# Optimization experiments

Hardware: AMD Instinct MI355X
Metric: run time of the kernel (lower is better)

Reference implementation:

```python
import jax, jax.numpy as jnp
import numpy as np

N = 100_000      # nodes
E = 1_600_000    # edges (avg degree 16)
IN, HID, OUT = 256, 256, 128  # in_dim, 2*out_dim, out_dim
BN_EPS = 1e-5


def setup_inputs() -> dict:
    key = jax.random.key(0)
    ks = jax.random.split(key, 8)
    x = jax.random.normal(ks[0], (N, IN), jnp.float32)
    edge_index = jax.random.randint(ks[1], (2, E), 0, N, dtype=jnp.int64)
    # GCNConv weights (glorot-ish scaling) + biases
    W1 = jax.random.normal(ks[2], (IN, HID), jnp.float32) * (1.0 / np.sqrt(IN))
    b1 = jnp.zeros((HID,), jnp.float32)
    W2 = jax.random.normal(ks[3], (HID, OUT), jnp.float32) * (1.0 / np.sqrt(HID))
    b2 = jnp.zeros((OUT,), jnp.float32)
    # BatchNorm1d affine params
    gamma = jnp.ones((HID,), jnp.float32)
    beta = jnp.zeros((HID,), jnp.float32)
    # PReLU single learnable slope (torch default 0.25)
    a = jnp.full((1,), 0.25, jnp.float32)
    return {"x": x, "edge_index": edge_index, "W1": W1, "b1": b1,
            "W2": W2, "b2": b2, "gamma": gamma, "beta": beta, "a": a}


def gcn_layer(x, W, b, src, dst):
    """GCNConv: h = D^-1/2 (A + I) D^-1/2 (x @ W) + b, self-loop weight 1."""
    h = x @ W                                           # [N, F]
    deg = jnp.zeros((N,), h.dtype).at[dst].add(1.0) + 1.0  # +1 self-loop
    dinv = jax.lax.rsqrt(deg)                           # [N]
    norm = dinv[src] * dinv[dst]                        # [E]
    agg = jnp.zeros_like(h).at[dst].add(h[src] * norm[:, None])
    agg = agg + h * (dinv * dinv)[:, None]              # self-loop term
    return agg + b


def reference(x, edge_index, W1, b1, W2, b2, gamma, beta, a):
    src, dst = edge_index[0], edge_index[1]
    h = gcn_layer(x, W1, b1, src, dst)                  # [N, HID]
    # BatchNorm1d (training mode: batch statistics, biased var)
    mean = jnp.mean(h, axis=0)
    var = jnp.var(h, axis=0)
    h = (h - mean) * jax.lax.rsqrt(var + BN_EPS) * gamma + beta
    # PReLU with single shared slope
    h = jnp.where(h > 0, h, a * h)
    return gcn_layer(h, W2, b2, src, dst)               # [N, OUT]
```

## Files before the change

kernel.cpp:

```cpp
#include <hip/hip_runtime.h>
#include <hip/hip_bf16.h>
#include <stdint.h>

#define IN_DIM 256

typedef __attribute__((ext_vector_type(8))) short short8;
typedef __attribute__((ext_vector_type(4))) float f32x4;

__device__ __forceinline__ float bf2f(unsigned short u){
  return __uint_as_float(((unsigned int)u) << 16);
}
__device__ __forceinline__ unsigned short f2bf(float f){
  unsigned int u = __float_as_uint(f);
  u = u + 0x7FFFu + ((u >> 16) & 1u);
  return (unsigned short)(u >> 16);
}
__device__ __forceinline__ int rfl(int v){ return __builtin_amdgcn_readfirstlane(v); }

#if __has_builtin(__builtin_amdgcn_cvt_f32_ubyte0)
__device__ __forceinline__ float ub0(uint v){ return __builtin_amdgcn_cvt_f32_ubyte0(v); }
__device__ __forceinline__ float ub1(uint v){ return __builtin_amdgcn_cvt_f32_ubyte1(v); }
__device__ __forceinline__ float ub2(uint v){ return __builtin_amdgcn_cvt_f32_ubyte2(v); }
__device__ __forceinline__ float ub3(uint v){ return __builtin_amdgcn_cvt_f32_ubyte3(v); }
#else
__device__ __forceinline__ float ub0(uint v){ return (float)(v & 0xFF); }
__device__ __forceinline__ float ub1(uint v){ return (float)((v >> 8) & 0xFF); }
__device__ __forceinline__ float ub2(uint v){ return (float)((v >> 16) & 0xFF); }
__device__ __forceinline__ float ub3(uint v){ return (float)(v >> 24); }
#endif

__global__ void k_detect(const void* ei, long long E, int N, int* flag){
  __shared__ int bad;
  if (threadIdx.x == 0) bad = 0;
  __syncthreads();
  const long long* p = (const long long*)ei;
  long long stride = E / 1024; if (stride < 1) stride = 1;
  for (int i = threadIdx.x; i < 1024; i += blockDim.x){
    long long idx = (long long)i * stride;
    if (idx >= E) break;
    long long v = p[idx];
    if (v < 0 || v >= (long long)N) atomicOr(&bad, 1);
  }
  __syncthreads();
  if (threadIdx.x == 0) flag[0] = bad ? 0 : 1;
}

__device__ __forceinline__ int edge_at(const void* ei, long long i, int f64){
  if (f64) return (int)((const long long*)ei)[i];
  return ((const int*)ei)[i];
}

__global__ void k_hist(const void* ei, long long E, const int* flag, int* cnt,
                       int* __restrict__ dst32, int* __restrict__ src32){
  long long e = (long long)blockIdx.x * blockDim.x + threadIdx.x;
  if (e < E){
    int f = flag[0];
    int s = edge_at(ei, e, f);
    int d = edge_at(ei, E + e, f);
    src32[e] = s;
    dst32[e] = d;
    atomicAdd(&cnt[d], 1);
  }
}

__global__ void k_scan1(const int* cnt, int* rs, int* bsum, float* dinv, int* fill, int N){
  __shared__ int sh[1024];
  int i = blockIdx.x * 1024 + threadIdx.x;
  int v = (i < N) ? cnt[i] : 0;
  sh[threadIdx.x] = v;
  __syncthreads();
  for (int o = 1; o < 1024; o <<= 1){
    int x = (threadIdx.x >= o) ? sh[threadIdx.x - o] : 0;
    __syncthreads();
    sh[threadIdx.x] += x;
    __syncthreads();
  }
  if (i < N){
    rs[i] = sh[threadIdx.x] - v;
    dinv[i] = rsqrtf((float)v + 1.0f);
    fill[i] = 0;
  }
  if (threadIdx.x == 1023) bsum[blockIdx.x] = sh[1023];
}

__global__ void k_scan2(const int* bsum, int* boff, int nb, int* rs, int N,
                        float* sums, float* sqs){
  __shared__ int sh[128];
  int t = threadIdx.x;
  int v = (t < nb) ? bsum[t] : 0;
  sh[t] = v;
  __syncthreads();
  for (int o = 1; o < 128; o <<= 1){
    int x = (t >= o) ? sh[t - o] : 0;
    __syncthreads();
    sh[t] += x;
    __syncthreads();
  }
  boff[t] = sh[t] - v;
  if (t == 127) rs[N] = sh[127];
  for (int j = t; j < 1024; j += 128){ sums[j] = 0.f; sqs[j] = 0.f; }
}

__global__ void k_scan3(int* rs, const int* boff, int N){
  int i = blockIdx.x * 1024 + threadIdx.x;
  if (i < N) rs[i] += boff[blockIdx.x];
}

__global__ __launch_bounds__(256) void k_scatter8(const int* __restrict__ dst32,
    const int* __restrict__ src32, long long E, const int* __restrict__ rs,
    int* __restrict__ fill, int* __restrict__ csrc, int N){
  const int g = blockIdx.x & 7;
  const int bg = blockIdx.x >> 3;
  const int Q = (N + 7) >> 3;
  const int lo = g * Q;
  const int hi = (lo + Q < N) ? lo + Q : N;
  const long long per = (E + 255) / 256;
  long long e0 = (long long)bg * per;
  long long e1 = e0 + per; if (e1 > E) e1 = E;
  for (long long e = e0 + threadIdx.x; e < e1; e += 256){
    int d = dst32[e];
    if (d >= lo && d < hi){
      int s = src32[e];
      int pos = atomicAdd(&fill[d], 1);
      csrc[rs[d] + pos] = s;
    }
  }
}

__global__ void k_prep(const float* __restrict__ x, ushort* __restrict__ xb,
                       const float* __restrict__ W1, ushort* __restrict__ W1t,
                       const float* __restrict__ W2, ushort* __restrict__ W2t,
                       int N, int NP){
  int idx = blockIdx.x * 256 + threadIdx.x;
  int nxq = NP * 64;
  if (idx < nxq){
    int row = idx >> 6, q = idx & 63;
    ushort4 o = {0, 0, 0, 0};
    if (row < N){
      float4 v = ((const float4*)x)[(size_t)row * 64 + q];
      o.x = f2bf(v.x); o.y = f2bf(v.y); o.z = f2bf(v.z); o.w = f2bf(v.w);
    }
    ((ushort4*)xb)[idx] = o;
  } else {
    int j = idx - nxq;
    if (j < 256 * 256){
      int n = j >> 8, k = j & 255;
      W1t[j] = f2bf(W1[(size_t)k * 256 + n]);
    } else {
      j -= 65536;
      if (j < 128 * 256){
        int n = j >> 8, k = j & 255;
        W2t[j] = f2bf(W2[(size_t)k * 128 + n]);
      }
    }
  }
}

__global__ __launch_bounds__(256, 2) void k_gemm1q(const ushort* __restrict__ A,
    const ushort* __restrict__ Bt, unsigned char* __restrict__ q8,
    float* __restrict__ sc1, const float* __restrict__ dinv, int N){
  __shared__ ushort As[128 * 64];
  __shared__ ushort Bs[256 * 64];
  __shared__ float smax[4][64];
  const int tid = threadIdx.x;
  const int wave = tid >> 6, lane = tid & 63;
  const long long row0 = (long long)blockIdx.x * 128;
  const int lr = lane >> 3, lc = lane & 7;
  const int mrow = ((wave & 1) << 6) + (lane & 15);
  const int ncb = ((wave >> 1) << 7) + (lane & 15);

  f32x4 acc[4][8];
  #pragma unroll
  for (int i = 0; i < 4; ++i)
    #pragma unroll
    for (int j = 0; j < 8; ++j)
      acc[i][j] = (f32x4){0.f, 0.f, 0.f, 0.f};

  const ushort* gA = A + (row0 + wave * 32 + lr) * 256 + lc * 8;
  const ushort* gB = Bt + (wave * 64 + lr) * 256 + lc * 8;
  ushort* lA = As + wave * 2048;
  ushort* lB = Bs + wave * 4096;

  #pragma unroll
  for (int kt = 0; kt < 4; ++kt){
    #pragma unroll
    for (int i = 0; i < 4; ++i)
      __builtin_amdgcn_global_load_lds(
          (const __attribute__((address_space(1))) void*)(gA + kt * 64 + i * 8 * 256),
          (__attribute__((address_space(3))) void*)(lA + i * 512), 16, 0, 0);
    #pragma unroll
    for (int i = 0; i < 8; ++i)
      __builtin_amdgcn_global_load_lds(
          (const __attribute__((address_space(1))) void*)(gB + kt * 64 + i * 8 * 256),
          (__attribute__((address_space(3))) void*)(lB + i * 512), 16, 0, 0);
    __syncthreads();
    #pragma unroll
    for (int ks = 0; ks < 2; ++ks){
      const int kb = ks * 32 + ((lane >> 4) << 3);
      short8 af[4], bfv[8];
      #pragma unroll
      for (int i = 0; i < 4; ++i) af[i] = *(const short8*)(As + (mrow + i * 16) * 64 + kb);
      #pragma unroll
      for (int j = 0; j < 8; ++j) bfv[j] = *(const short8*)(Bs + (ncb + j * 16) * 64 + kb);
      #pragma unroll
      for (int i = 0; i < 4; ++i)
        #pragma unroll
        for (int j = 0; j < 8; ++j)
          acc[i][j] = __builtin_amdgcn_mfma_f32_16x16x32_bf16(af[i], bfv[j], acc[i][j], 0, 0, 0);
    }
    __syncthreads();
  }

  const int rbase = ((wave & 1) << 6) + ((lane >> 4) << 2);
  float m[4][4];
  #pragma unroll
  for (int i = 0; i < 4; ++i)
    #pragma unroll
    for (int r = 0; r < 4; ++r){
      long long row = row0 + rbase + i * 16 + r;
      float dv = (row < N) ? dinv[row] : 0.f;
      float mm = 0.f;
      #pragma unroll
      for (int j = 0; j < 8; ++j){
        float v = dv * acc[i][j][r];
        acc[i][j][r] = v;
        mm = fmaxf(mm, fabsf(v));
      }
      #pragma unroll
      for (int o = 8; o >= 1; o >>= 1) mm = fmaxf(mm, __shfl_xor(mm, o, 16));
      m[i][r] = mm;
    }
  if ((lane & 15) == 0){
    #pragma unroll
    for (int i = 0; i < 4; ++i)
      #pragma unroll
      for (int r = 0; r < 4; ++r)
        smax[wave][((lane >> 4) << 2) + i * 16 + r] = m[i][r];
  }
  __syncthreads();
  #pragma unroll
  for (int i = 0; i < 4; ++i)
    #pragma unroll
    for (int r = 0; r < 4; ++r){
      int rh = ((lane >> 4) << 2) + i * 16 + r;
      long long row = row0 + ((wave & 1) << 6) + rh;
      float mm = fmaxf(m[i][r], smax[wave ^ 2][rh]);
      float inv = (mm > 0.f) ? 127.0f / mm : 0.f;
      if (wave < 2 && (lane & 15) == 0 && row < N) sc1[row] = mm * (1.0f / 127.0f);
      #pragma unroll
      for (int j = 0; j < 8; ++j){
        unsigned char b = (unsigned char)(int)(rintf(acc[i][j][r] * inv) + 128.0f);
        q8[(size_t)row * 256 + ncb + j * 16] = b;
      }
    }
}

__global__ __launch_bounds__(256) void k_gemm2q(const ushort* __restrict__ A,
    const ushort* __restrict__ Bt, unsigned char* __restrict__ q8,
    float* __restrict__ sc2, const float* __restrict__ dinv, int N){
  __shared__ ushort As[128 * 64];
  __shared__ ushort Bs[128 * 64];
  __shared__ float smax[4][64];
  const int tid = threadIdx.x;
  const int wave = tid >> 6, lane = tid & 63;
  const long long row0 = (long long)blockIdx.x * 128;
  const int lr = lane >> 3, lc = lane & 7;
  const int mrow = ((wave & 1) << 6) + (lane & 15);
  const int ncol = ((wave >> 1) << 6) + (lane & 15);

  f32x4 acc[4][4];
  #pragma unroll
  for (int i = 0; i < 4; ++i)
    #pragma unroll
    for (int j = 0; j < 4; ++j)
      acc[i][j] = (f32x4){0.f, 0.f, 0.f, 0.f};

  const ushort* gA = A + (row0 + wave * 32 + lr) * 256 + lc * 8;
  const ushort* gB = Bt + ((long long)(wave * 32 + lr)) * 256 + lc * 8;
  ushort* lA = As + wave * 2048;
  ushort* lB = Bs + wave * 2048;

  #pragma unroll
  for (int kt = 0; kt < 4; ++kt){
    #pragma unroll
    for (int i = 0; i < 4; ++i){
      __builtin_amdgcn_global_load_lds(
          (const __attribute__((address_space(1))) void*)(gA + kt * 64 + i * 8 * 256),
          (__attribute__((address_space(3))) void*)(lA + i * 512), 16, 0, 0);
      __builtin_amdgcn_global_load_lds(
          (const __attribute__((address_space(1))) void*)(gB + kt * 64 + i * 8 * 256),
          (__attribute__((address_space(3))) void*)(lB + i * 512), 16, 0, 0);
    }
    __syncthreads();
    #pragma unroll
    for (int ks = 0; ks < 2; ++ks){
      const int kb = ks * 32 + ((lane >> 4) << 3);
      short8 af[4], bfv[4];
      #pragma unroll
      for (int i = 0; i < 4; ++i) af[i] = *(const short8*)(As + (mrow + i * 16) * 64 + kb);
      #pragma unroll
      for (int j = 0; j < 4; ++j) bfv[j] = *(const short8*)(Bs + (ncol + j * 16) * 64 + kb);
      #pragma unroll
      for (int i = 0; i < 4; ++i)
        #pragma unroll
        for (int j = 0; j < 4; ++j)
          acc[i][j] = __builtin_amdgcn_mfma_f32_16x16x32_bf16(af[i], bfv[j], acc[i][j], 0, 0, 0);
    }
    __syncthreads();
  }

  const int rbase = ((wave & 1) << 6) + ((lane >> 4) << 2);
  const int cb = ((wave >> 1) << 6) + (lane & 15);
  float m[4][4];
  #pragma unroll
  for (int i = 0; i < 4; ++i)
    #pragma unroll
    for (int r = 0; r < 4; ++r){
      long long row = row0 + rbase + i * 16 + r;
      float dv = (row < N) ? dinv[row] : 0.f;
      float mm = 0.f;
      #pragma unroll
      for (int j = 0; j < 4; ++j){
        float v = dv * acc[i][j][r];
        acc[i][j][r] = v;
        mm = fmaxf(mm, fabsf(v));
      }
      #pragma unroll
      for (int o = 8; o >= 1; o >>= 1) mm = fmaxf(mm, __shfl_xor(mm, o, 16));
      m[i][r] = mm;
    }
  if ((lane & 15) == 0){
    #pragma unroll
    for (int i = 0; i < 4; ++i)
      #pragma unroll
      for (int r = 0; r < 4; ++r)
        smax[wave][((lane >> 4) << 2) + i * 16 + r] = m[i][r];
  }
  __syncthreads();
  #pragma unroll
  for (int i = 0; i < 4; ++i)
    #pragma unroll
    for (int r = 0; r < 4; ++r){
      int rh = ((lane >> 4) << 2) + i * 16 + r;
      long long row = row0 + ((wave & 1) << 6) + rh;
      float mm = fmaxf(m[i][r], smax[wave ^ 2][rh]);
      float inv = (mm > 0.f) ? 127.0f / mm : 0.f;
      if (wave < 2 && (lane & 15) == 0 && row < N) sc2[row] = mm * (1.0f / 127.0f);
      #pragma unroll
      for (int j = 0; j < 4; ++j){
        unsigned char b = (unsigned char)(int)(rintf(acc[i][j][r] * inv) + 128.0f);
        q8[(size_t)row * 128 + cb + j * 16] = b;
      }
    }
}

__global__ __launch_bounds__(256) void k_agg1(const uint* __restrict__ q, const float* __restrict__ sc,
    const int* __restrict__ rs, const int* __restrict__ csrc, const float* __restrict__ b1,
    ushort* __restrict__ h1, float* __restrict__ sums, float* __restrict__ sqs,
    int N, int nblocks){
  __shared__ float red[4 * 512];
  const int lane = threadIdx.x & 63;
  const int wid = rfl((blockIdx.x * 256 + threadIdx.x) >> 6);
  const int nw = (nblocks * 256) >> 6;
  const float4 bb = ((const float4*)b1)[lane];
  const uint* ql = q + lane;
  float st0 = 0.f, st1 = 0.f, st2 = 0.f, st3 = 0.f;
  float sq0 = 0.f, sq1 = 0.f, sq2 = 0.f, sq3 = 0.f;

  for (int n = wid; n < N; n += nw){
    int e = rfl(rs[n]), end = rfl(rs[n + 1]);
    float dn = rsqrtf((float)(end - e) + 1.0f);
    float scn = sc[n];
    uint v = ql[(uint)n << 6];
    float ssum = scn;
    float a0 = scn * ub0(v), a1 = scn * ub1(v), a2 = scn * ub2(v), a3 = scn * ub3(v);
    for (; e + 8 <= end; e += 8){
      int s0 = rfl(csrc[e]),     s1 = rfl(csrc[e + 1]), s2 = rfl(csrc[e + 2]), s3 = rfl(csrc[e + 3]);
      int s4 = rfl(csrc[e + 4]), s5 = rfl(csrc[e + 5]), s6 = rfl(csrc[e + 6]), s7 = rfl(csrc[e + 7]);
      float c0 = sc[s0], c1 = sc[s1], c2 = sc[s2], c3 = sc[s3];
      float c4 = sc[s4], c5 = sc[s5], c6 = sc[s6], c7 = sc[s7];
      uint v0 = ql[(uint)s0 << 6];
      uint v1 = ql[(uint)s1 << 6];
      uint v2 = ql[(uint)s2 << 6];
      uint v3 = ql[(uint)s3 << 6];
      uint v4 = ql[(uint)s4 << 6];
      uint v5 = ql[(uint)s5 << 6];
      uint v6 = ql[(uint)s6 << 6];
      uint v7 = ql[(uint)s7 << 6];
      ssum += ((c0 + c1) + (c2 + c3)) + ((c4 + c5) + (c6 + c7));
      a0 += ((c0 * ub0(v0) + c1 * ub0(v1)) + (c2 * ub0(v2) + c3 * ub0(v3)))
          + ((c4 * ub0(v4) + c5 * ub0(v5)) + (c6 * ub0(v6) + c7 * ub0(v7)));
      a1 += ((c0 * ub1(v0) + c1 * ub1(v1)) + (c2 * ub1(v2) + c3 * ub1(v3)))
          + ((c4 * ub1(v4) + c5 * ub1(v5)) + (c6 * ub1(v6) + c7 * ub1(v7)));
      a2 += ((c0 * ub2(v0) + c1 * ub2(v1)) + (c2 * ub2(v2) + c3 * ub2(v3)))
          + ((c4 * ub2(v4) + c5 * ub2(v5)) + (c6 * ub2(v6) + c7 * ub2(v7)));
      a3 += ((c0 * ub3(v0) + c1 * ub3(v1)) + (c2 * ub3(v2) + c3 * ub3(v3)))
          + ((c4 * ub3(v4) + c5 * ub3(v5)) + (c6 * ub3(v6) + c7 * ub3(v7)));
    }
    for (; e + 4 <= end; e += 4){
      int s0 = rfl(csrc[e]), s1 = rfl(csrc[e + 1]), s2 = rfl(csrc[e + 2]), s3 = rfl(csrc[e + 3]);
      float c0 = sc[s0], c1 = sc[s1], c2 = sc[s2], c3 = sc[s3];
      uint v0 = ql[(uint)s0 << 6];
      uint v1 = ql[(uint)s1 << 6];
      uint v2 = ql[(uint)s2 << 6];
      uint v3 = ql[(uint)s3 << 6];
      ssum += (c0 + c1) + (c2 + c3);
      a0 += (c0 * ub0(v0) + c1 * ub0(v1)) + (c2 * ub0(v2) + c3 * ub0(v3));
      a1 += (c0 * ub1(v0) + c1 * ub1(v1)) + (c2 * ub1(v2) + c3 * ub1(v3));
      a2 += (c0 * ub2(v0) + c1 * ub2(v1)) + (c2 * ub2(v2) + c3 * ub2(v3));
      a3 += (c0 * ub3(v0) + c1 * ub3(v1)) + (c2 * ub3(v2) + c3 * ub3(v3));
    }
    for (; e < end; ++e){
      int s = rfl(csrc[e]);
      float c = sc[s];
      uint vv = ql[(uint)s << 6];
      ssum += c;
      a0 += c * ub0(vv); a1 += c * ub1(vv); a2 += c * ub2(vv); a3 += c * ub3(vv);
    }
    float corr = -128.0f * ssum;
    float h0 = dn * (a0 + corr) + bb.x;
    float h1v = dn * (a1 + corr) + bb.y;
    float h2 = dn * (a2 + corr) + bb.z;
    float h3 = dn * (a3 + corr) + bb.w;
    st0 += h0; st1 += h1v; st2 += h2; st3 += h3;
    sq0 += h0 * h0; sq1 += h1v * h1v; sq2 += h2 * h2; sq3 += h3 * h3;
    ushort4 o;
    o.x = f2bf(h0); o.y = f2bf(h1v); o.z = f2bf(h2); o.w = f2bf(h3);
    ((ushort4*)h1)[(size_t)n * 64 + lane] = o;
  }

  int wv = threadIdx.x >> 6;
  int f = lane * 4;
  red[wv * 512 + f]     = st0; red[wv * 512 + f + 1] = st1;
  red[wv * 512 + f + 2] = st2; red[wv * 512 + f + 3] = st3;
  __syncthreads();
  float v0s = red[threadIdx.x] + red[512 + threadIdx.x] + red[1024 + threadIdx.x] + red[1536 + threadIdx.x];
  __syncthreads();
  red[wv * 512 + f]     = sq0; red[wv * 512 + f + 1] = sq1;
  red[wv * 512 + f + 2] = sq2; red[wv * 512 + f + 3] = sq3;
  __syncthreads();
  float v0q = red[threadIdx.x] + red[512 + threadIdx.x] + red[1024 + threadIdx.x] + red[1536 + threadIdx.x];
  if (threadIdx.x < 256){
    int rep = ((blockIdx.x & 3) << 8) + threadIdx.x;
    atomicAdd(&sums[rep], v0s);
    atomicAdd(&sqs[rep], v0q);
  }
}

__global__ __launch_bounds__(256) void k_agg2(const ushort* __restrict__ q, const float* __restrict__ sc,
    const int* __restrict__ rs, const int* __restrict__ csrc, const float* __restrict__ b2,
    float* __restrict__ out, int N, int nblocks){
  const int lane = threadIdx.x & 63;
  const int wid = rfl((blockIdx.x * 256 + threadIdx.x) >> 6);
  const int nw = (nblocks * 256) >> 6;
  const float2 bb = ((const float2*)b2)[lane];
  const ushort* ql = q + lane;

  for (int n = wid; n < N; n += nw){
    int e = rfl(rs[n]), end = rfl(rs[n + 1]);
    float dn = rsqrtf((float)(end - e) + 1.0f);
    float scn = sc[n];
    uint v = (uint)ql[(uint)n << 6];
    float ssum = scn;
    float a0 = scn * ub0(v), a1 = scn * ub1(v);
    for (; e + 8 <= end; e += 8){
      int s0 = rfl(csrc[e]),     s1 = rfl(csrc[e + 1]), s2 = rfl(csrc[e + 2]), s3 = rfl(csrc[e + 3]);
      int s4 = rfl(csrc[e + 4]), s5 = rfl(csrc[e + 5]), s6 = rfl(csrc[e + 6]), s7 = rfl(csrc[e + 7]);
      float c0 = sc[s0], c1 = sc[s1], c2 = sc[s2], c3 = sc[s3];
      float c4 = sc[s4], c5 = sc[s5], c6 = sc[s6], c7 = sc[s7];
      uint v0 = (uint)ql[(uint)s0 << 6];
      uint v1 = (uint)ql[(uint)s1 << 6];
      uint v2 = (uint)ql[(uint)s2 << 6];
      uint v3 = (uint)ql[(uint)s3 << 6];
      uint v4 = (uint)ql[(uint)s4 << 6];
      uint v5 = (uint)ql[(uint)s5 << 6];
      uint v6 = (uint)ql[(uint)s6 << 6];
      uint v7 = (uint)ql[(uint)s7 << 6];
      ssum += ((c0 + c1) + (c2 + c3)) + ((c4 + c5) + (c6 + c7));
      a0 += ((c0 * ub0(v0) + c1 * ub0(v1)) + (c2 * ub0(v2) + c3 * ub0(v3)))
          + ((c4 * ub0(v4) + c5 * ub0(v5)) + (c6 * ub0(v6) + c7 * ub0(v7)));
      a1 += ((c0 * ub1(v0) + c1 * ub1(v1)) + (c2 * ub1(v2) + c3 * ub1(v3)))
          + ((c4 * ub1(v4) + c5 * ub1(v5)) + (c6 * ub1(v6) + c7 * ub1(v7)));
    }
    for (; e + 4 <= end; e += 4){
      int s0 = rfl(csrc[e]), s1 = rfl(csrc[e + 1]), s2 = rfl(csrc[e + 2]), s3 = rfl(csrc[e + 3]);
      float c0 = sc[s0], c1 = sc[s1], c2 = sc[s2], c3 = sc[s3];
      uint v0 = (uint)ql[(uint)s0 << 6];
      uint v1 = (uint)ql[(uint)s1 << 6];
      uint v2 = (uint)ql[(uint)s2 << 6];
      uint v3 = (uint)ql[(uint)s3 << 6];
      ssum += (c0 + c1) + (c2 + c3);
      a0 += (c0 * ub0(v0) + c1 * ub0(v1)) + (c2 * ub0(v2) + c3 * ub0(v3));
      a1 += (c0 * ub1(v0) + c1 * ub1(v1)) + (c2 * ub1(v2) + c3 * ub1(v3));
    }
    for (; e < end; ++e){
      int s = rfl(csrc[e]);
      float c = sc[s];
      uint vv = (uint)ql[(uint)s << 6];
      ssum += c;
      a0 += c * ub0(vv); a1 += c * ub1(vv);
    }
    float corr = -128.0f * ssum;
    float2 r;
    r.x = dn * (a0 + corr) + bb.x;
    r.y = dn * (a1 + corr) + bb.y;
    ((float2*)out)[(size_t)n * 64 + lane] = r;
  }
}

__global__ void k_prelu(const ushort* __restrict__ h1, const float* __restrict__ sums,
                        const float* __restrict__ sqs, const float* __restrict__ gamma,
                        const float* __restrict__ beta, const float* __restrict__ aP,
                        ushort* __restrict__ P, int N, int NP){
  int idx = blockIdx.x * 256 + threadIdx.x;
  int row = idx >> 7, cp = idx & 127;
  if (row >= NP) return;
  uint o = 0;
  if (row < N){
    int c0 = 2 * cp;
    float inv = 1.0f / (float)N;
    float s0 = sums[c0]     + sums[256 + c0]     + sums[512 + c0]     + sums[768 + c0];
    float s1 = sums[c0 + 1] + sums[256 + c0 + 1] + sums[512 + c0 + 1] + sums[768 + c0 + 1];
    float q0 = sqs[c0]      + sqs[256 + c0]      + sqs[512 + c0]      + sqs[768 + c0];
    float q1 = sqs[c0 + 1]  + sqs[256 + c0 + 1]  + sqs[512 + c0 + 1]  + sqs[768 + c0 + 1];
    float m0 = s0 * inv,     m1 = s1 * inv;
    float v0 = q0 * inv - m0 * m0, v1 = q1 * inv - m1 * m1;
    float sc0 = gamma[c0] * rsqrtf(v0 + 1e-5f);
    float sc1 = gamma[c0 + 1] * rsqrtf(v1 + 1e-5f);
    float sh0 = beta[c0] - m0 * sc0;
    float sh1 = beta[c0 + 1] - m1 * sc1;
    uint v = ((const uint*)h1)[(size_t)row * 128 + cp];
    float aa = aP[0];
    float x0 = bf2f((unsigned short)(v & 0xFFFF)) * sc0 + sh0;
    float x1 = bf2f((unsigned short)(v >> 16)) * sc1 + sh1;
    x0 = x0 > 0.f ? x0 : aa * x0;
    x1 = x1 > 0.f ? x1 : aa * x1;
    o = (uint)f2bf(x0) | ((uint)f2bf(x1) << 16);
  }
  ((uint*)P)[idx] = o;
}

extern "C" void kernel_launch(void* const* d_in, const int* in_sizes, int n_in,
                              void* d_out, int out_size, void* d_ws, size_t ws_size,
                              hipStream_t stream){
  const float* x  = (const float*)d_in[0];
  const void*  ei = d_in[1];
  const float* W1 = (const float*)d_in[2];
  const float* b1 = (const float*)d_in[3];
  const float* W2 = (const float*)d_in[4];
  const float* b2 = (const float*)d_in[5];
  const float* gm = (const float*)d_in[6];
  const float* bt = (const float*)d_in[7];
  const float* aP = (const float*)d_in[8];
  float* out = (float*)d_out;

  const int N = in_sizes[0] / IN_DIM;
  const long long E = in_sizes[1] / 2;
  const int NP = ((N + 127) / 128) * 128;

  char* w = (char*)d_ws;
  size_t off = 0;
  auto carve = [&](size_t bytes) -> char* {
    char* p = w + off;
    off += (bytes + 255) & ~(size_t)255;
    return p;
  };
  ushort* xb  = (ushort*)carve((size_t)NP * 256 * 2);
  ushort* hb  = (ushort*)carve((size_t)NP * 256 * 2);
  ushort* h1b = (ushort*)carve((size_t)NP * 256 * 2);
  ushort* W1t = (ushort*)carve(256 * 256 * 2);
  ushort* W2t = (ushort*)carve(128 * 256 * 2);
  int*   cnt  = (int*)  carve((size_t)N * 4);
  int*   rs   = (int*)  carve((size_t)(N + 1) * 4);
  int*   fill = (int*)  carve((size_t)N * 4);
  int*   csrc = (int*)  carve((size_t)E * 4);
  float* dinv = (float*)carve((size_t)N * 4);
  float* sc1  = (float*)carve((size_t)N * 4);
  float* sc2  = (float*)carve((size_t)N * 4);
  int*   bsum = (int*)  carve(512);
  int*   boff = (int*)  carve(512);
  float* sums = (float*)carve(4096);
  float* sqs  = (float*)carve(4096);
  int*   flag = (int*)  carve(256);
  int*   dst32 = (int*)hb;
  int*   src32 = ((int*)hb) + E;
  uint*   q8a = (uint*)hb;
  ushort* q8b = (ushort*)h1b;

  const int NB1 = (N + 1023) / 1024;
  const int egrid = (int)((E + 255) / 256);
  const int prep_grid = (NP * 64 + 256 * 256 + 128 * 256 + 255) / 256;
  const int AGG1_BLOCKS = 2048, AGG2_BLOCKS = 2048;

  k_detect<<<1, 256, 0, stream>>>(ei, E, N, flag);
  hipMemsetAsync(cnt, 0, (size_t)N * 4, stream);
  k_prep<<<prep_grid, 256, 0, stream>>>(x, xb, W1, W1t, W2, W2t, N, NP);
  k_hist<<<egrid, 256, 0, stream>>>(ei, E, flag, cnt, dst32, src32);
  k_scan1<<<NB1, 1024, 0, stream>>>(cnt, rs, bsum, dinv, fill, N);
  k_scan2<<<1, 128, 0, stream>>>(bsum, boff, NB1, rs, N, sums, sqs);
  k_scan3<<<NB1, 1024, 0, stream>>>(rs, boff, N);
  k_scatter8<<<2048, 256, 0, stream>>>(dst32, src32, E, rs, fill, csrc, N);

  k_gemm1q<<<NP / 128, 256, 0, stream>>>(xb, W1t, (unsigned char*)q8a, sc1, dinv, N);
  k_agg1<<<AGG1_BLOCKS, 256, 0, stream>>>(q8a, sc1, rs, csrc, b1, h1b, sums, sqs, N, AGG1_BLOCKS);
  k_prelu<<<(NP * 128 + 255) / 256, 256, 0, stream>>>(h1b, sums, sqs, gm, bt, aP, xb, N, NP);
  k_gemm2q<<<NP / 128, 256, 0, stream>>>(xb, W2t, (unsigned char*)q8b, sc2, dinv, N);
  k_agg2<<<AGG2_BLOCKS, 256, 0, stream>>>(q8b, sc2, rs, csrc, b2, out, N, AGG2_BLOCKS);
}
```

Baseline: 580.9 us.

## Fuse fp32-to-bf16 conversion of x into GEMM1 and use FMA chains in aggregation

```diff
diff --git a/kernel.cpp b/kernel.cpp
--- a/kernel.cpp
+++ b/kernel.cpp
@@ -127,36 +127,22 @@
   }
 }
 
-__global__ void k_prep(const float* __restrict__ x, ushort* __restrict__ xb,
-                       const float* __restrict__ W1, ushort* __restrict__ W1t,
-                       const float* __restrict__ W2, ushort* __restrict__ W2t,
-                       int N, int NP){
-  int idx = blockIdx.x * 256 + threadIdx.x;
-  int nxq = NP * 64;
-  if (idx < nxq){
-    int row = idx >> 6, q = idx & 63;
-    ushort4 o = {0, 0, 0, 0};
-    if (row < N){
-      float4 v = ((const float4*)x)[(size_t)row * 64 + q];
-      o.x = f2bf(v.x); o.y = f2bf(v.y); o.z = f2bf(v.z); o.w = f2bf(v.w);
-    }
-    ((ushort4*)xb)[idx] = o;
+__global__ void k_prepw(const float* __restrict__ W1, ushort* __restrict__ W1t,
+                        const float* __restrict__ W2, ushort* __restrict__ W2t){
+  int j = blockIdx.x * 256 + threadIdx.x;
+  if (j < 256 * 256){
+    int n = j >> 8, k = j & 255;
+    W1t[j] = f2bf(W1[(size_t)k * 256 + n]);
   } else {
-    int j = idx - nxq;
-    if (j < 256 * 256){
-      int n = j >> 8, k = j & 255;
-      W1t[j] = f2bf(W1[(size_t)k * 256 + n]);
-    } else {
-      j -= 65536;
-      if (j < 128 * 256){
-        int n = j >> 8, k = j & 255;
-        W2t[j] = f2bf(W2[(size_t)k * 128 + n]);
-      }
-    }
-  }
-}
-
-__global__ __launch_bounds__(256, 2) void k_gemm1q(const ushort* __restrict__ A,
+    int j2 = j - 65536;
+    if (j2 < 128 * 256){
+      int n = j2 >> 8, k = j2 & 255;
+      W2t[j2] = f2bf(W2[(size_t)k * 128 + n]);
+    }
+  }
+}
+
+__global__ __launch_bounds__(256, 2) void k_gemm1q(const float* __restrict__ X,
     const ushort* __restrict__ Bt, unsigned char* __restrict__ q8,
     float* __restrict__ sc1, const float* __restrict__ dinv, int N){
   __shared__ ushort As[128 * 64];
@@ -166,6 +152,7 @@
   const int wave = tid >> 6, lane = tid & 63;
   const long long row0 = (long long)blockIdx.x * 128;
   const int lr = lane >> 3, lc = lane & 7;
+  const int sr = lane >> 4, scq = lane & 15;
   const int mrow = ((wave & 1) << 6) + (lane & 15);
   const int ncb = ((wave >> 1) << 7) + (lane & 15);
 
@@ -176,23 +163,27 @@
     for (int j = 0; j < 8; ++j)
       acc[i][j] = (f32x4){0.f, 0.f, 0.f, 0.f};
 
-  const ushort* gA = A + (row0 + wave * 32 + lr) * 256 + lc * 8;
   const ushort* gB = Bt + (wave * 64 + lr) * 256 + lc * 8;
-  ushort* lA = As + wave * 2048;
   ushort* lB = Bs + wave * 4096;
 
   #pragma unroll
   for (int kt = 0; kt < 4; ++kt){
-    #pragma unroll
-    for (int i = 0; i < 4; ++i)
-      __builtin_amdgcn_global_load_lds(
-          (const __attribute__((address_space(1))) void*)(gA + kt * 64 + i * 8 * 256),
-          (__attribute__((address_space(3))) void*)(lA + i * 512), 16, 0, 0);
     #pragma unroll
     for (int i = 0; i < 8; ++i)
       __builtin_amdgcn_global_load_lds(
           (const __attribute__((address_space(1))) void*)(gB + kt * 64 + i * 8 * 256),
           (__attribute__((address_space(3))) void*)(lB + i * 512), 16, 0, 0);
+    #pragma unroll
+    for (int p = 0; p < 8; ++p){
+      int rl = wave * 32 + p * 4 + sr;
+      long long grow = row0 + rl;
+      float4 xv = {0.f, 0.f, 0.f, 0.f};
+      if (grow < N) xv = *(const float4*)(X + grow * 256 + kt * 64 + scq * 4);
+      uint2 wv;
+      wv.x = (uint)f2bf(xv.x) | ((uint)f2bf(xv.y) << 16);
+      wv.y = (uint)f2bf(xv.z) | ((uint)f2bf(xv.w) << 16);
+      *(uint2*)(As + rl * 64 + scq * 4) = wv;
+    }
     __syncthreads();
     #pragma unroll
     for (int ks = 0; ks < 2; ++ks){
@@ -388,14 +379,22 @@
       uint v6 = ql[(uint)s6 << 6];
       uint v7 = ql[(uint)s7 << 6];
       ssum += ((c0 + c1) + (c2 + c3)) + ((c4 + c5) + (c6 + c7));
-      a0 += ((c0 * ub0(v0) + c1 * ub0(v1)) + (c2 * ub0(v2) + c3 * ub0(v3)))
-          + ((c4 * ub0(v4) + c5 * ub0(v5)) + (c6 * ub0(v6) + c7 * ub0(v7)));
-      a1 += ((c0 * ub1(v0) + c1 * ub1(v1)) + (c2 * ub1(v2) + c3 * ub1(v3)))
-          + ((c4 * ub1(v4) + c5 * ub1(v5)) + (c6 * ub1(v6) + c7 * ub1(v7)));
-      a2 += ((c0 * ub2(v0) + c1 * ub2(v1)) + (c2 * ub2(v2) + c3 * ub2(v3)))
-          + ((c4 * ub2(v4) + c5 * ub2(v5)) + (c6 * ub2(v6) + c7 * ub2(v7)));
-      a3 += ((c0 * ub3(v0) + c1 * ub3(v1)) + (c2 * ub3(v2) + c3 * ub3(v3)))
-          + ((c4 * ub3(v4) + c5 * ub3(v5)) + (c6 * ub3(v6) + c7 * ub3(v7)));
+      a0 = fmaf(c0, ub0(v0), a0); a0 = fmaf(c1, ub0(v1), a0);
+      a0 = fmaf(c2, ub0(v2), a0); a0 = fmaf(c3, ub0(v3), a0);
+      a0 = fmaf(c4, ub0(v4), a0); a0 = fmaf(c5, ub0(v5), a0);
+      a0 = fmaf(c6, ub0(v6), a0); a0 = fmaf(c7, ub0(v7), a0);
+      a1 = fmaf(c0, ub1(v0), a1); a1 = fmaf(c1, ub1(v1), a1);
+      a1 = fmaf(c2, ub1(v2), a1); a1 = fmaf(c3, ub1(v3), a1);
+      a1 = fmaf(c4, ub1(v4), a1); a1 = fmaf(c5, ub1(v5), a1);
+      a1 = fmaf(c6, ub1(v6), a1); a1 = fmaf(c7, ub1(v7), a1);
+      a2 = fmaf(c0, ub2(v0), a2); a2 = fmaf(c1, ub2(v1), a2);
+      a2 = fmaf(c2, ub2(v2), a2); a2 = fmaf(c3, ub2(v3), a2);
+      a2 = fmaf(c4, ub2(v4), a2); a2 = fmaf(c5, ub2(v5), a2);
+      a2 = fmaf(c6, ub2(v6), a2); a2 = fmaf(c7, ub2(v7), a2);
+      a3 = fmaf(c0, ub3(v0), a3); a3 = fmaf(c1, ub3(v1), a3);
+      a3 = fmaf(c2, ub3(v2), a3); a3 = fmaf(c3, ub3(v3), a3);
+      a3 = fmaf(c4, ub3(v4), a3); a3 = fmaf(c5, ub3(v5), a3);
+      a3 = fmaf(c6, ub3(v6), a3); a3 = fmaf(c7, ub3(v7), a3);
     }
     for (; e + 4 <= end; e += 4){
       int s0 = rfl(csrc[e]), s1 = rfl(csrc[e + 1]), s2 = rfl(csrc[e + 2]), s3 = rfl(csrc[e + 3]);
@@ -405,17 +404,22 @@
       uint v2 = ql[(uint)s2 << 6];
       uint v3 = ql[(uint)s3 << 6];
       ssum += (c0 + c1) + (c2 + c3);
-      a0 += (c0 * ub0(v0) + c1 * ub0(v1)) + (c2 * ub0(v2) + c3 * ub0(v3));
-      a1 += (c0 * ub1(v0) + c1 * ub1(v1)) + (c2 * ub1(v2) + c3 * ub1(v3));
-      a2 += (c0 * ub2(v0) + c1 * ub2(v1)) + (c2 * ub2(v2) + c3 * ub2(v3));
-      a3 += (c0 * ub3(v0) + c1 * ub3(v1)) + (c2 * ub3(v2) + c3 * ub3(v3));
+      a0 = fmaf(c0, ub0(v0), a0); a0 = fmaf(c1, ub0(v1), a0);
+      a0 = fmaf(c2, ub0(v2), a0); a0 = fmaf(c3, ub0(v3), a0);
+      a1 = fmaf(c0, ub1(v0), a1); a1 = fmaf(c1, ub1(v1), a1);
+      a1 = fmaf(c2, ub1(v2), a1); a1 = fmaf(c3, ub1(v3), a1);
+      a2 = fmaf(c0, ub2(v0), a2); a2 = fmaf(c1, ub2(v1), a2);
+      a2 = fmaf(c2, ub2(v2), a2); a2 = fmaf(c3, ub2(v3), a2);
+      a3 = fmaf(c0, ub3(v0), a3); a3 = fmaf(c1, ub3(v1), a3);
+      a3 = fmaf(c2, ub3(v2), a3); a3 = fmaf(c3, ub3(v3), a3);
     }
     for (; e < end; ++e){
       int s = rfl(csrc[e]);
       float c = sc[s];
       uint vv = ql[(uint)s << 6];
       ssum += c;
-      a0 += c * ub0(vv); a1 += c * ub1(vv); a2 += c * ub2(vv); a3 += c * ub3(vv);
+      a0 = fmaf(c, ub0(vv), a0); a1 = fmaf(c, ub1(vv), a1);
+      a2 = fmaf(c, ub2(vv), a2); a3 = fmaf(c, ub3(vv), a3);
     }
     float corr = -128.0f * ssum;
     float h0 = dn * (a0 + corr) + bb.x;
@@ -477,10 +481,14 @@
       uint v6 = (uint)ql[(uint)s6 << 6];
       uint v7 = (uint)ql[(uint)s7 << 6];
       ssum += ((c0 + c1) + (c2 + c3)) + ((c4 + c5) + (c6 + c7));
-      a0 += ((c0 * ub0(v0) + c1 * ub0(v1)) + (c2 * ub0(v2) + c3 * ub0(v3)))
-          + ((c4 * ub0(v4) + c5 * ub0(v5)) + (c6 * ub0(v6) + c7 * ub0(v7)));
-      a1 += ((c0 * ub1(v0) + c1 * ub1(v1)) + (c2 * ub1(v2) + c3 * ub1(v3)))
-          + ((c4 * ub1(v4) + c5 * ub1(v5)) + (c6 * ub1(v6) + c7 * ub1(v7)));
+      a0 = fmaf(c0, ub0(v0), a0); a0 = fmaf(c1, ub0(v1), a0);
+      a0 = fmaf(c2, ub0(v2), a0); a0 = fmaf(c3, ub0(v3), a0);
+      a0 = fmaf(c4, ub0(v4), a0); a0 = fmaf(c5, ub0(v5), a0);
+      a0 = fmaf(c6, ub0(v6), a0); a0 = fmaf(c7, ub0(v7), a0);
+      a1 = fmaf(c0, ub1(v0), a1); a1 = fmaf(c1, ub1(v1), a1);
+      a1 = fmaf(c2, ub1(v2), a1); a1 = fmaf(c3, ub1(v3), a1);
+      a1 = fmaf(c4, ub1(v4), a1); a1 = fmaf(c5, ub1(v5), a1);
+      a1 = fmaf(c6, ub1(v6), a1); a1 = fmaf(c7, ub1(v7), a1);
     }
     for (; e + 4 <= end; e += 4){
       int s0 = rfl(csrc[e]), s1 = rfl(csrc[e + 1]), s2 = rfl(csrc[e + 2]), s3 = rfl(csrc[e + 3]);
@@ -490,15 +498,17 @@
       uint v2 = (uint)ql[(uint)s2 << 6];
       uint v3 = (uint)ql[(uint)s3 << 6];
       ssum += (c0 + c1) + (c2 + c3);
-      a0 += (c0 * ub0(v0) + c1 * ub0(v1)) + (c2 * ub0(v2) + c3 * ub0(v3));
-      a1 += (c0 * ub1(v0) + c1 * ub1(v1)) + (c2 * ub1(v2) + c3 * ub1(v3));
+      a0 = fmaf(c0, ub0(v0), a0); a0 = fmaf(c1, ub0(v1), a0);
+      a0 = fmaf(c2, ub0(v2), a0); a0 = fmaf(c3, ub0(v3), a0);
+      a1 = fmaf(c0, ub1(v0), a1); a1 = fmaf(c1, ub1(v1), a1);
+      a1 = fmaf(c2, ub1(v2), a1); a1 = fmaf(c3, ub1(v3), a1);
     }
     for (; e < end; ++e){
       int s = rfl(csrc[e]);
       float c = sc[s];
       uint vv = (uint)ql[(uint)s << 6];
       ssum += c;
-      a0 += c * ub0(vv); a1 += c * ub1(vv);
+      a0 = fmaf(c, ub0(vv), a0); a1 = fmaf(c, ub1(vv), a1);
     }
     float corr = -128.0f * ssum;
     float2 r;
@@ -589,19 +599,18 @@
 
   const int NB1 = (N + 1023) / 1024;
   const int egrid = (int)((E + 255) / 256);
-  const int prep_grid = (NP * 64 + 256 * 256 + 128 * 256 + 255) / 256;
   const int AGG1_BLOCKS = 2048, AGG2_BLOCKS = 2048;
 
   k_detect<<<1, 256, 0, stream>>>(ei, E, N, flag);
   hipMemsetAsync(cnt, 0, (size_t)N * 4, stream);
-  k_prep<<<prep_grid, 256, 0, stream>>>(x, xb, W1, W1t, W2, W2t, N, NP);
+  k_prepw<<<384, 256, 0, stream>>>(W1, W1t, W2, W2t);
   k_hist<<<egrid, 256, 0, stream>>>(ei, E, flag, cnt, dst32, src32);
   k_scan1<<<NB1, 1024, 0, stream>>>(cnt, rs, bsum, dinv, fill, N);
   k_scan2<<<1, 128, 0, stream>>>(bsum, boff, NB1, rs, N, sums, sqs);
   k_scan3<<<NB1, 1024, 0, stream>>>(rs, boff, N);
   k_scatter8<<<2048, 256, 0, stream>>>(dst32, src32, E, rs, fill, csrc, N);
 
-  k_gemm1q<<<NP / 128, 256, 0, stream>>>(xb, W1t, (unsigned char*)q8a, sc1, dinv, N);
+  k_gemm1q<<<NP / 128, 256, 0, stream>>>(x, W1t, (unsigned char*)q8a, sc1, dinv, N);
   k_agg1<<<AGG1_BLOCKS, 256, 0, stream>>>(q8a, sc1, rs, csrc, b1, h1b, sums, sqs, N, AGG1_BLOCKS);
   k_prelu<<<(NP * 128 + 255) / 256, 256, 0, stream>>>(h1b, sums, sqs, gm, bt, aP, xb, N, NP);
   k_gemm2q<<<NP / 128, 256, 0, stream>>>(xb, W2t, (unsigned char*)q8b, sc2, dinv, N);
```

Result: no change. 587.4 us (+1.1%).
